# Optimization experiments

Hardware: AMD Instinct MI355X
Metric: run time of the kernel (lower is better)

The kernel has to match this reference:

```python
import jax, jax.numpy as jnp
import numpy as np

N, K = 524288, 128

def setup_inputs() -> dict:
    key = jax.random.key(0)
    k1, k2 = jax.random.split(key)
    inputs = jax.random.normal(k1, (N, K), dtype=jnp.float32)
    target = jax.random.uniform(k2, (N, K), dtype=jnp.float32)
    return {"input": inputs, "target": target}

def reference(input, target):
    # Equivalent to: for each class y, cum += target[:, y] * cross_entropy(input, y)
    # cross_entropy(input, y) = -log_softmax(input)[:, y], so the loop reduces to a
    # single log_softmax and a weighted row-sum against the target probabilities.
    log_p = jax.nn.log_softmax(input, axis=-1)          # [n, k]
    cum_losses = -jnp.sum(target * log_p, axis=-1)       # [n]
    return jnp.mean(cum_losses)                          # reduction='mean'
```

## Files before the change

kernel.cpp:

```cpp
#include <hip/hip_runtime.h>
#include <math.h>


#define KDIM 128
#define BLOCK 256
#define GRID 2048
#define UNROLL 4

typedef float v4f __attribute__((ext_vector_type(4)));

__global__ __launch_bounds__(BLOCK) void sce_partial_kernel(
    const float* __restrict__ x, const float* __restrict__ t,
    float* __restrict__ partials, int n_rows) {
    const int tid  = threadIdx.x;
    const int lane = tid & 63;
    const int sub  = lane & 31;
    const int half = lane >> 5;
    const int wave_in_block = tid >> 6;
    const int wave_id = blockIdx.x * (BLOCK / 64) + wave_in_block;
    const int n_waves = GRID * (BLOCK / 64);
    const int n_pairs = n_rows >> 1;

    float acc = 0.0f;

    int p0 = wave_id * UNROLL;
    const int stride = n_waves * UNROLL;
    for (; p0 + UNROLL <= n_pairs; p0 += stride) {
        v4f xv[UNROLL], tv[UNROLL];
        #pragma unroll
        for (int u = 0; u < UNROLL; ++u) {
            const size_t row_off =
                ((size_t)(p0 + u) * 2 + half) * KDIM + sub * 4;
            xv[u] = __builtin_nontemporal_load(
                        reinterpret_cast<const v4f*>(x + row_off));
            tv[u] = __builtin_nontemporal_load(
                        reinterpret_cast<const v4f*>(t + row_off));
        }

        float e[UNROLL];
        #pragma unroll
        for (int u = 0; u < UNROLL; ++u)
            e[u] = __expf(xv[u].x) + __expf(xv[u].y) +
                   __expf(xv[u].z) + __expf(xv[u].w);

        #pragma unroll
        for (int off = 16; off >= 1; off >>= 1) {
            #pragma unroll
            for (int u = 0; u < UNROLL; ++u)
                e[u] += __shfl_xor(e[u], off, 64);
        }

        #pragma unroll
        for (int u = 0; u < UNROLL; ++u) {
            const float ts = tv[u].x + tv[u].y + tv[u].z + tv[u].w;
            float dt = tv[u].x * xv[u].x;
            dt = fmaf(tv[u].y, xv[u].y, dt);
            dt = fmaf(tv[u].z, xv[u].z, dt);
            dt = fmaf(tv[u].w, xv[u].w, dt);
            acc += fmaf(ts, __logf(e[u]), -dt);
        }
    }

    for (; p0 < n_pairs; ++p0) {
        const size_t row_off = ((size_t)p0 * 2 + half) * KDIM + sub * 4;
        const v4f xv = __builtin_nontemporal_load(
                           reinterpret_cast<const v4f*>(x + row_off));
        const v4f tv = __builtin_nontemporal_load(
                           reinterpret_cast<const v4f*>(t + row_off));
        float e = __expf(xv.x) + __expf(xv.y) + __expf(xv.z) + __expf(xv.w);
        #pragma unroll
        for (int off = 16; off >= 1; off >>= 1)
            e += __shfl_xor(e, off, 64);
        const float ts = tv.x + tv.y + tv.z + tv.w;
        const float dt = tv.x * xv.x + tv.y * xv.y + tv.z * xv.z + tv.w * xv.w;
        acc += ts * __logf(e) - dt;
    }

    #pragma unroll
    for (int off = 32; off >= 1; off >>= 1)
        acc += __shfl_xor(acc, off, 64);

    __shared__ float ws[BLOCK / 64];
    if (lane == 0) ws[wave_in_block] = acc;
    __syncthreads();
    if (tid == 0) {
        float s = 0.0f;
        #pragma unroll
        for (int i = 0; i < BLOCK / 64; ++i) s += ws[i];
        partials[blockIdx.x] = s;
    }
}

__global__ __launch_bounds__(256) void sce_finalize_kernel(
    const float* __restrict__ partials, float* __restrict__ out,
    int n_partials, float inv_n) {
    float s = 0.0f;
    for (int i = threadIdx.x; i < n_partials; i += 256) s += partials[i];
    #pragma unroll
    for (int off = 32; off >= 1; off >>= 1) s += __shfl_xor(s, off, 64);
    __shared__ float ws[4];
    const int lane = threadIdx.x & 63, w = threadIdx.x >> 6;
    if (lane == 0) ws[w] = s;
    __syncthreads();
    if (threadIdx.x == 0) {
        float tot = 0.0f;
        #pragma unroll
        for (int i = 0; i < 4; ++i) tot += ws[i];
        out[0] = tot * inv_n;
    }
}

extern "C" void kernel_launch(void* const* d_in, const int* in_sizes, int n_in,
                              void* d_out, int out_size, void* d_ws, size_t ws_size,
                              hipStream_t stream) {
    const float* x = (const float*)d_in[0];
    const float* t = (const float*)d_in[1];
    float* out = (float*)d_out;
    float* partials = (float*)d_ws;

    const int n_rows = in_sizes[0] / KDIM;

    sce_partial_kernel<<<GRID, BLOCK, 0, stream>>>(x, t, partials, n_rows);
    sce_finalize_kernel<<<1, 256, 0, stream>>>(partials, out, GRID,
                                               1.0f / (float)n_rows);
}
```

Before: 467.7 us.

## Give each wave a contiguous row range and double-buffer register loads

Each wave now processes a contiguous block of row pairs instead of a grid-strided interleaving, and loads for the next batch are issued into a second register set before computing the current one (software pipelining). The grid shrinks to 1280 blocks with a launch-bounds occupancy hint of 5 blocks per CU, and the per-lane sum order is rebalanced. The intent is to keep more memory requests in flight per wave on a bandwidth-bound kernel, at the cost of doubled register footprint for the buffers and possible load imbalance from the contiguous split.

```diff
diff --git a/kernel.cpp b/kernel.cpp
--- a/kernel.cpp
+++ b/kernel.cpp
@@ -4,44 +4,54 @@
 
 #define KDIM 128
 #define BLOCK 256
-#define GRID 2048
+#define GRID 1280
 #define UNROLL 4
 
 typedef float v4f __attribute__((ext_vector_type(4)));
 
-__global__ __launch_bounds__(BLOCK) void sce_partial_kernel(
+__global__ __launch_bounds__(BLOCK, 5) void sce_partial_kernel(
     const float* __restrict__ x, const float* __restrict__ t,
     float* __restrict__ partials, int n_rows) {
     const int tid  = threadIdx.x;
     const int lane = tid & 63;
-    const int sub  = lane & 31;
-    const int half = lane >> 5;
     const int wave_in_block = tid >> 6;
     const int wave_id = blockIdx.x * (BLOCK / 64) + wave_in_block;
     const int n_waves = GRID * (BLOCK / 64);
     const int n_pairs = n_rows >> 1;
 
+    const int ppw   = n_pairs / n_waves;
+    const int extra = n_pairs - ppw * n_waves;
+    const int p_begin = wave_id * ppw + (wave_id < extra ? wave_id : extra);
+    const int count   = ppw + (wave_id < extra ? 1 : 0);
+
+    const size_t base = (size_t)p_begin * (2 * KDIM) + (size_t)lane * 4;
+    const float* xp = x + base;
+    const float* tp = t + base;
+
     float acc = 0.0f;
 
-    int p0 = wave_id * UNROLL;
-    const int stride = n_waves * UNROLL;
-    for (; p0 + UNROLL <= n_pairs; p0 += stride) {
-        v4f xv[UNROLL], tv[UNROLL];
+    const int nb = count / UNROLL;
+
+    v4f xa[UNROLL], ta[UNROLL], xb[UNROLL], tb[UNROLL];
+
+    auto load_batch = [&](v4f* xv, v4f* tv, int b) {
+        const float* xq = xp + (size_t)b * (UNROLL * 2 * KDIM);
+        const float* tq = tp + (size_t)b * (UNROLL * 2 * KDIM);
         #pragma unroll
         for (int u = 0; u < UNROLL; ++u) {
-            const size_t row_off =
-                ((size_t)(p0 + u) * 2 + half) * KDIM + sub * 4;
             xv[u] = __builtin_nontemporal_load(
-                        reinterpret_cast<const v4f*>(x + row_off));
+                        reinterpret_cast<const v4f*>(xq + u * (2 * KDIM)));
             tv[u] = __builtin_nontemporal_load(
-                        reinterpret_cast<const v4f*>(t + row_off));
+                        reinterpret_cast<const v4f*>(tq + u * (2 * KDIM)));
         }
+    };
 
+    auto compute_batch = [&](const v4f* xv, const v4f* tv) {
         float e[UNROLL];
         #pragma unroll
         for (int u = 0; u < UNROLL; ++u)
-            e[u] = __expf(xv[u].x) + __expf(xv[u].y) +
-                   __expf(xv[u].z) + __expf(xv[u].w);
+            e[u] = (__expf(xv[u].x) + __expf(xv[u].y)) +
+                   (__expf(xv[u].z) + __expf(xv[u].w));
 
         #pragma unroll
         for (int off = 16; off >= 1; off >>= 1) {
@@ -52,26 +62,44 @@
 
         #pragma unroll
         for (int u = 0; u < UNROLL; ++u) {
-            const float ts = tv[u].x + tv[u].y + tv[u].z + tv[u].w;
+            const float ts = (tv[u].x + tv[u].y) + (tv[u].z + tv[u].w);
             float dt = tv[u].x * xv[u].x;
             dt = fmaf(tv[u].y, xv[u].y, dt);
             dt = fmaf(tv[u].z, xv[u].z, dt);
             dt = fmaf(tv[u].w, xv[u].w, dt);
             acc += fmaf(ts, __logf(e[u]), -dt);
         }
+    };
+
+    if (nb > 0) {
+        load_batch(xa, ta, 0);
+        int b = 1;
+        for (; b + 1 < nb; b += 2) {
+            load_batch(xb, tb, b);
+            compute_batch(xa, ta);
+            load_batch(xa, ta, b + 1);
+            compute_batch(xb, tb);
+        }
+        if (b < nb) {
+            load_batch(xb, tb, b);
+            compute_batch(xa, ta);
+            compute_batch(xb, tb);
+        } else {
+            compute_batch(xa, ta);
+        }
     }
 
-    for (; p0 < n_pairs; ++p0) {
-        const size_t row_off = ((size_t)p0 * 2 + half) * KDIM + sub * 4;
+    for (int p = p_begin + nb * UNROLL; p < p_begin + count; ++p) {
+        const size_t off = (size_t)p * (2 * KDIM) + (size_t)lane * 4;
         const v4f xv = __builtin_nontemporal_load(
-                           reinterpret_cast<const v4f*>(x + row_off));
+                           reinterpret_cast<const v4f*>(x + off));
         const v4f tv = __builtin_nontemporal_load(
-                           reinterpret_cast<const v4f*>(t + row_off));
-        float e = __expf(xv.x) + __expf(xv.y) + __expf(xv.z) + __expf(xv.w);
+                           reinterpret_cast<const v4f*>(t + off));
+        float e = (__expf(xv.x) + __expf(xv.y)) + (__expf(xv.z) + __expf(xv.w));
         #pragma unroll
-        for (int off = 16; off >= 1; off >>= 1)
-            e += __shfl_xor(e, off, 64);
-        const float ts = tv.x + tv.y + tv.z + tv.w;
+        for (int o = 16; o >= 1; o >>= 1)
+            e += __shfl_xor(e, o, 64);
+        const float ts = (tv.x + tv.y) + (tv.z + tv.w);
         const float dt = tv.x * xv.x + tv.y * xv.y + tv.z * xv.z + tv.w * xv.w;
         acc += ts * __logf(e) - dt;
     }
```

New measurement: 495.3 us. 1.06x slower.
